# Kernel optimization log

Measured on AMD Instinct MI355X. Metric: run time of the kernel, lower is better.

Reference implementation:

```python
import jax, jax.numpy as jnp
import numpy as np

WINDOW_SIZE = 11
CHANNEL = 1
SIGMA = 1.5


def _gaussian_window(window_size=WINDOW_SIZE, channel=CHANNEL, sigma=SIGMA):
    x = np.arange(window_size)
    g = np.exp(-((x - window_size // 2) ** 2) / (2.0 * sigma ** 2))
    g = g / g.sum()
    w2d = np.outer(g, g).astype(np.float32)  # [K,K]
    # depthwise conv kernel: [C_out=channel, C_in/groups=1, K, K]
    return jnp.asarray(np.broadcast_to(w2d, (channel, 1, window_size, window_size)))


def _dwconv(x, window):
    pad = WINDOW_SIZE // 2
    return jax.lax.conv_general_dilated(
        x, window,
        window_strides=(1, 1),
        padding=[(pad, pad), (pad, pad)],
        dimension_numbers=('NCHW', 'OIHW', 'NCHW'),
        feature_group_count=CHANNEL)


def _ssim(img1, img2, window):
    C1 = 0.01 ** 2
    C2 = 0.03 ** 2
    mu1 = _dwconv(img1, window)
    mu2 = _dwconv(img2, window)
    mu1_sq = mu1 * mu1
    mu2_sq = mu2 * mu2
    mu1_mu2 = mu1 * mu2
    sigma1_sq = _dwconv(img1 * img1, window) - mu1_sq
    sigma2_sq = _dwconv(img2 * img2, window) - mu2_sq
    sigma12 = _dwconv(img1 * img2, window) - mu1_mu2
    ssim_map = ((2.0 * mu1_mu2 + C1) * (2.0 * sigma12 + C2)) / (
        (mu1_sq + mu2_sq + C1) * (sigma1_sq + sigma2_sq + C2))
    return ssim_map.mean()


def setup_inputs() -> dict:
    key = jax.random.key(0)
    k1, k2 = jax.random.split(key)
    B, C, H, W = 64, 1, 512, 512
    pred = jax.random.uniform(k1, (B, C, H, W), dtype=jnp.float32)
    target = jax.random.uniform(k2, (B, C, H, W), dtype=jnp.float32)
    return {"pred": pred, "target": target}


def reference(pred, target):
    window = _gaussian_window()
    return 1.0 - _ssim(pred[:, :1], target[:, :1], window)
```

## Files before the change

kernel.cpp:

```cpp
#include <hip/hip_runtime.h>

#define BATCH 64
#define HH 512
#define WW 512
#define TH 32
#define KS 11
#define PADK 5
#define NIN (TH + 2 * PADK)
#define NF4 262
#define NPIX (64.0 * 512.0 * 512.0)

__global__ void __launch_bounds__(256, 2) ssim_main_kernel(
    const float* __restrict__ img1, const float* __restrict__ img2,
    double* __restrict__ accum) {
  constexpr float GA[KS] = {
      0.00102838f, 0.00759884f, 0.03600087f, 0.10936069f, 0.21300553f,
      0.26601172f, 0.21300553f, 0.10936069f, 0.03600087f, 0.00759884f,
      0.00102838f};
  const float C1v = 1e-4f, C2v = 9e-4f;

  const int t  = threadIdx.x;
  const int r0 = blockIdx.x * TH;
  const int b  = blockIdx.y;

  const float2* __restrict__ pp1 =
      reinterpret_cast<const float2*>(img1 + (size_t)b * HH * WW);
  const float2* __restrict__ pp2 =
      reinterpret_cast<const float2*>(img2 + (size_t)b * HH * WW);

  __shared__ float4 sh[2][4][NF4];
  __shared__ float wsum[4];

  if (t < 6) {
    const int idx = (t < 3) ? t : (256 + t);
#pragma unroll
    for (int bi = 0; bi < 2; ++bi)
#pragma unroll
      for (int r = 0; r < 4; ++r) sh[bi][r][idx] = make_float4(0.f, 0.f, 0.f, 0.f);
  }

#define DECLR(s) float xA##s = 0.f, xB##s = 0.f, xQ##s = 0.f, xP##s = 0.f, \
                       yA##s = 0.f, yB##s = 0.f, yQ##s = 0.f, yP##s = 0.f;
  DECLR(0) DECLR(1) DECLR(2) DECLR(3) DECLR(4) DECLR(5)
  DECLR(6) DECLR(7) DECLR(8) DECLR(9) DECLR(10)

  float2 ta0, ta1, ta2, ta3, tb0, tb1, tb2, tb3;
  float local = 0.f;

#define LD1(k_, j_)                                                     \
  {                                                                     \
    constexpr int rc_ = 4 * (k_) + (j_);                                \
    ta##j_ = make_float2(0.f, 0.f);                                     \
    tb##j_ = make_float2(0.f, 0.f);                                     \
    if constexpr (rc_ < NIN) {                                          \
      const int rr_ = r0 - PADK + rc_;                                  \
      if ((unsigned)rr_ < HH) {                                         \
        const int off_ = rr_ * (WW / 2) + t;                            \
        ta##j_ = pp1[off_];                                             \
        tb##j_ = pp2[off_];                                             \
      }                                                                 \
    }                                                                   \
  }
#define LOADC(k_) { LD1(k_, 0) LD1(k_, 1) LD1(k_, 2) LD1(k_, 3) }

#define WR1(k_, j_)                                                     \
  {                                                                     \
    constexpr int rc_ = 4 * (k_) + (j_);                                \
    if constexpr (rc_ < NIN)                                            \
      sh[(k_) & 1][j_][t + 3] =                                         \
          make_float4(ta##j_.x, tb##j_.x, ta##j_.y, tb##j_.y);          \
  }
#define WRITEC(k_) { WR1(k_, 0) WR1(k_, 1) WR1(k_, 2) WR1(k_, 3) }

#define HBODY(B_, j_, S)                                                      \
  {                                                                           \
    float h0a = 0.f, h0b = 0.f, h0q = 0.f, h0p = 0.f;                         \
    float h1a = 0.f, h1b = 0.f, h1q = 0.f, h1p = 0.f;                         \
    _Pragma("unroll")                                                         \
    for (int kk = 0; kk < 7; ++kk) {                                          \
      const float4 v = sh[B_][j_][t + kk];                                    \
      if (kk >= 1) {                         \
        const float qv_ = fmaf(v.x, v.x, v.y * v.y);                          \
        const float pv_ = v.x * v.y;                                          \
        if (kk <= 5) {                                                        \
          const float w = GA[2 * kk - 1];                                     \
          h0a = fmaf(w, v.x, h0a); h0b = fmaf(w, v.y, h0b);                   \
          h0q = fmaf(w, qv_, h0q); h0p = fmaf(w, pv_, h0p);                   \
        }                                                                     \
        {                                                                     \
          const float w = GA[2 * kk - 2];                                     \
          h1a = fmaf(w, v.x, h1a); h1b = fmaf(w, v.y, h1b);                   \
          h1q = fmaf(w, qv_, h1q); h1p = fmaf(w, pv_, h1p);                   \
        }                                                                     \
      }                                                                       \
      if (kk <= 5) {                           \
        const float qv_ = fmaf(v.z, v.z, v.w * v.w);                          \
        const float pv_ = v.z * v.w;                                          \
        {                                                                     \
          const float w = GA[2 * kk];                                         \
          h0a = fmaf(w, v.z, h0a); h0b = fmaf(w, v.w, h0b);                   \
          h0q = fmaf(w, qv_, h0q); h0p = fmaf(w, pv_, h0p);                   \
        }                                                                     \
        if (kk >= 1) {                                                        \
          const float w = GA[2 * kk - 1];                                     \
          h1a = fmaf(w, v.z, h1a); h1b = fmaf(w, v.w, h1b);                   \
          h1q = fmaf(w, qv_, h1q); h1p = fmaf(w, pv_, h1p);                   \
        }                                                                     \
      }                                                                       \
    }                                                                         \
    xA##S = h0a; xB##S = h0b; xQ##S = h0q; xP##S = h0p;                       \
    yA##S = h1a; yB##S = h1b; yQ##S = h1q; yP##S = h1p;                       \
  }

#define VC(P, s0,s1,s2v,s3,s4v,s5,s6v,s7,s8,s9,s10)                           \
  fmaf(GA[10], P##s10, fmaf(GA[9], P##s9, fmaf(GA[8], P##s8,                  \
  fmaf(GA[7], P##s7, fmaf(GA[6], P##s6v, fmaf(GA[5], P##s5,                   \
  fmaf(GA[4], P##s4v, fmaf(GA[3], P##s3, fmaf(GA[2], P##s2v,                  \
  fmaf(GA[1], P##s1, GA[0] * P##s0))))))))))

#define SSIMACC                                                               \
  {                                                                           \
    const float m1s = m1 * m1, m2s = m2 * m2, m12 = m1 * m2;                  \
    const float s12 = mp - m12;                                               \
    const float sqq = mq - m1s - m2s;                                         \
    const float num = fmaf(2.f, m12, C1v) * fmaf(2.f, s12, C2v);              \
    const float den = (m1s + m2s + C1v) * (sqq + C2v);                        \
    local = fmaf(num, __builtin_amdgcn_rcpf(den), local);                     \
  }

#define VOUTBODY(s0,s1,s2v,s3,s4v,s5,s6v,s7,s8,s9,s10)                        \
  {                                                                           \
    {                                                                         \
      const float m1 = VC(xA, s0,s1,s2v,s3,s4v,s5,s6v,s7,s8,s9,s10);          \
      const float m2 = VC(xB, s0,s1,s2v,s3,s4v,s5,s6v,s7,s8,s9,s10);          \
      const float mq = VC(xQ, s0,s1,s2v,s3,s4v,s5,s6v,s7,s8,s9,s10);          \
      const float mp = VC(xP, s0,s1,s2v,s3,s4v,s5,s6v,s7,s8,s9,s10);          \
      SSIMACC                                                                 \
    }                                                                         \
    {                                                                         \
      const float m1 = VC(yA, s0,s1,s2v,s3,s4v,s5,s6v,s7,s8,s9,s10);          \
      const float m2 = VC(yB, s0,s1,s2v,s3,s4v,s5,s6v,s7,s8,s9,s10);          \
      const float mq = VC(yQ, s0,s1,s2v,s3,s4v,s5,s6v,s7,s8,s9,s10);          \
      const float mp = VC(yP, s0,s1,s2v,s3,s4v,s5,s6v,s7,s8,s9,s10);          \
      SSIMACC                                                                 \
    }                                                                         \
  }

#define ROT0  0,1,2,3,4,5,6,7,8,9,10
#define ROT1  1,2,3,4,5,6,7,8,9,10,0
#define ROT2  2,3,4,5,6,7,8,9,10,0,1
#define ROT3  3,4,5,6,7,8,9,10,0,1,2
#define ROT4  4,5,6,7,8,9,10,0,1,2,3
#define ROT5  5,6,7,8,9,10,0,1,2,3,4
#define ROT6  6,7,8,9,10,0,1,2,3,4,5
#define ROT7  7,8,9,10,0,1,2,3,4,5,6
#define ROT8  8,9,10,0,1,2,3,4,5,6,7
#define ROT9  9,10,0,1,2,3,4,5,6,7,8
#define ROT10 10,0,1,2,3,4,5,6,7,8,9
#define VOUTE(...) VOUTBODY(__VA_ARGS__)

#define ROWH(B_, j_, S)        { HBODY(B_, j_, S) }
#define ROWO(B_, j_, S, R_)    { HBODY(B_, j_, S) VOUTE(R_) }

  LOADC(0) WRITEC(0) LOADC(1)
  __syncthreads();

  WRITEC(1) LOADC(2)
  ROWH(0,0,0) ROWH(0,1,1) ROWH(0,2,2) ROWH(0,3,3)
  __syncthreads();
  WRITEC(2) LOADC(3)
  ROWH(1,0,4) ROWH(1,1,5) ROWH(1,2,6) ROWH(1,3,7)
  __syncthreads();
  WRITEC(3) LOADC(4)
  ROWH(0,0,8) ROWH(0,1,9)
  ROWO(0,2,10, ROT0) ROWO(0,3,0, ROT1)
  __syncthreads();
  WRITEC(4) LOADC(5)
  ROWO(1,0,1, ROT2) ROWO(1,1,2, ROT3) ROWO(1,2,3, ROT4) ROWO(1,3,4, ROT5)
  __syncthreads();
  WRITEC(5) LOADC(6)
  ROWO(0,0,5, ROT6) ROWO(0,1,6, ROT7) ROWO(0,2,7, ROT8) ROWO(0,3,8, ROT9)
  __syncthreads();
  WRITEC(6) LOADC(7)
  ROWO(1,0,9, ROT10) ROWO(1,1,10, ROT0) ROWO(1,2,0, ROT1) ROWO(1,3,1, ROT2)
  __syncthreads();
  WRITEC(7) LOADC(8)
  ROWO(0,0,2, ROT3) ROWO(0,1,3, ROT4) ROWO(0,2,4, ROT5) ROWO(0,3,5, ROT6)
  __syncthreads();
  WRITEC(8) LOADC(9)
  ROWO(1,0,6, ROT7) ROWO(1,1,7, ROT8) ROWO(1,2,8, ROT9) ROWO(1,3,9, ROT10)
  __syncthreads();
  WRITEC(9) LOADC(10)
  ROWO(0,0,10, ROT0) ROWO(0,1,0, ROT1) ROWO(0,2,1, ROT2) ROWO(0,3,2, ROT3)
  __syncthreads();
  WRITEC(10)
  ROWO(1,0,3, ROT4) ROWO(1,1,4, ROT5) ROWO(1,2,5, ROT6) ROWO(1,3,6, ROT7)
  __syncthreads();
  ROWO(0,0,7, ROT8) ROWO(0,1,8, ROT9)

#pragma unroll
  for (int off = 32; off > 0; off >>= 1) local += __shfl_down(local, off, 64);
  const int wave = t >> 6;
  const int lane = t & 63;
  if (lane == 0) wsum[wave] = local;
  __syncthreads();
  if (t == 0) {
    float s = wsum[0] + wsum[1] + wsum[2] + wsum[3];
    atomicAdd(accum, (double)s);
  }
}

__global__ void ssim_final_kernel(const double* __restrict__ accum,
                                  float* __restrict__ out) {
  out[0] = 1.0f - (float)(accum[0] / NPIX);
}

extern "C" void kernel_launch(void* const* d_in, const int* in_sizes, int n_in,
                              void* d_out, int out_size, void* d_ws, size_t ws_size,
                              hipStream_t stream) {
  const float* img1 = (const float*)d_in[0];
  const float* img2 = (const float*)d_in[1];
  double* accum = (double*)d_ws;
  hipMemsetAsync(accum, 0, sizeof(double), stream);

  dim3 grid(HH / TH, BATCH);
  ssim_main_kernel<<<grid, 256, 0, stream>>>(img1, img2, accum);
  ssim_final_kernel<<<1, 1, 0, stream>>>(accum, (float*)d_out);
}
```

Measured before the change: 212.2 us.

## Give each wave a private shared-memory tile with halo to drop block barriers

The shared-memory staging buffer is split into per-wave slices of 64+6 float4 entries. Six lanes per wave load and write their own halo columns. With each wave producing and consuming only its own slice, all the __syncthreads calls in the row pipeline are removed and only the final reduction barrier stays. This relies on in-order LDS access within a single wave. The cost is extra halo global loads, a slightly larger LDS footprint and extra per-lane branching.

```diff
diff --git a/kernel.cpp b/kernel.cpp
--- a/kernel.cpp
+++ b/kernel.cpp
@@ -7,7 +7,7 @@
 #define KS 11
 #define PADK 5
 #define NIN (TH + 2 * PADK)
-#define NF4 262
+#define WS4 70
 #define NPIX (64.0 * 512.0 * 512.0)
 
 __global__ void __launch_bounds__(256, 2) ssim_main_kernel(
@@ -20,6 +20,8 @@
   const float C1v = 1e-4f, C2v = 9e-4f;
 
   const int t  = threadIdx.x;
+  const int l  = t & 63;
+  const int w  = t >> 6;
   const int r0 = blockIdx.x * TH;
   const int b  = blockIdx.y;
 
@@ -28,16 +30,12 @@
   const float2* __restrict__ pp2 =
       reinterpret_cast<const float2*>(img2 + (size_t)b * HH * WW);
 
-  __shared__ float4 sh[2][4][NF4];
+  __shared__ float4 sh[4][2][4][WS4];
   __shared__ float wsum[4];
 
-  if (t < 6) {
-    const int idx = (t < 3) ? t : (256 + t);
-#pragma unroll
-    for (int bi = 0; bi < 2; ++bi)
-#pragma unroll
-      for (int r = 0; r < 4; ++r) sh[bi][r][idx] = make_float4(0.f, 0.f, 0.f, 0.f);
-  }
+  const int  hs   = (l < 3) ? l : (l + 64);
+  const int  hidx = 64 * w + hs - 3;
+  const bool hval = (l < 6) && ((unsigned)hidx < (unsigned)(WW / 2));
 
 #define DECLR(s) float xA##s = 0.f, xB##s = 0.f, xQ##s = 0.f, xP##s = 0.f, \
                        yA##s = 0.f, yB##s = 0.f, yQ##s = 0.f, yP##s = 0.f;
@@ -45,19 +43,24 @@
   DECLR(6) DECLR(7) DECLR(8) DECLR(9) DECLR(10)
 
   float2 ta0, ta1, ta2, ta3, tb0, tb1, tb2, tb3;
+  float2 ha0, ha1, ha2, ha3, hb0, hb1, hb2, hb3;
   float local = 0.f;
 
 #define LD1(k_, j_)                                                     \
   {                                                                     \
     constexpr int rc_ = 4 * (k_) + (j_);                                \
-    ta##j_ = make_float2(0.f, 0.f);                                     \
-    tb##j_ = make_float2(0.f, 0.f);                                     \
+    ta##j_ = make_float2(0.f, 0.f); tb##j_ = make_float2(0.f, 0.f);     \
+    ha##j_ = make_float2(0.f, 0.f); hb##j_ = make_float2(0.f, 0.f);     \
     if constexpr (rc_ < NIN) {                                          \
       const int rr_ = r0 - PADK + rc_;                                  \
       if ((unsigned)rr_ < HH) {                                         \
-        const int off_ = rr_ * (WW / 2) + t;                            \
-        ta##j_ = pp1[off_];                                             \
-        tb##j_ = pp2[off_];                                             \
+        const int off_ = rr_ * (WW / 2);                                \
+        ta##j_ = pp1[off_ + t];                                         \
+        tb##j_ = pp2[off_ + t];                                         \
+        if (hval) {                                                     \
+          ha##j_ = pp1[off_ + hidx];                                    \
+          hb##j_ = pp2[off_ + hidx];                                    \
+        }                                                               \
       }                                                                 \
     }                                                                   \
   }
@@ -66,9 +69,13 @@
 #define WR1(k_, j_)                                                     \
   {                                                                     \
     constexpr int rc_ = 4 * (k_) + (j_);                                \
-    if constexpr (rc_ < NIN)                                            \
-      sh[(k_) & 1][j_][t + 3] =                                         \
+    if constexpr (rc_ < NIN) {                                          \
+      sh[w][(k_) & 1][j_][l + 3] =                                      \
           make_float4(ta##j_.x, tb##j_.x, ta##j_.y, tb##j_.y);          \
+      if (l < 6)                                                        \
+        sh[w][(k_) & 1][j_][hs] =                                       \
+            make_float4(ha##j_.x, hb##j_.x, ha##j_.y, hb##j_.y);        \
+    }                                                                   \
   }
 #define WRITEC(k_) { WR1(k_, 0) WR1(k_, 1) WR1(k_, 2) WR1(k_, 3) }
 
@@ -78,33 +85,33 @@
     float h1a = 0.f, h1b = 0.f, h1q = 0.f, h1p = 0.f;                         \
     _Pragma("unroll")                                                         \
     for (int kk = 0; kk < 7; ++kk) {                                          \
-      const float4 v = sh[B_][j_][t + kk];                                    \
+      const float4 v = sh[w][B_][j_][l + kk];                                 \
       if (kk >= 1) {                         \
         const float qv_ = fmaf(v.x, v.x, v.y * v.y);                          \
         const float pv_ = v.x * v.y;                                          \
         if (kk <= 5) {                                                        \
-          const float w = GA[2 * kk - 1];                                     \
-          h0a = fmaf(w, v.x, h0a); h0b = fmaf(w, v.y, h0b);                   \
-          h0q = fmaf(w, qv_, h0q); h0p = fmaf(w, pv_, h0p);                   \
+          const float w_ = GA[2 * kk - 1];                                    \
+          h0a = fmaf(w_, v.x, h0a); h0b = fmaf(w_, v.y, h0b);                 \
+          h0q = fmaf(w_, qv_, h0q); h0p = fmaf(w_, pv_, h0p);                 \
         }                                                                     \
         {                                                                     \
-          const float w = GA[2 * kk - 2];                                     \
-          h1a = fmaf(w, v.x, h1a); h1b = fmaf(w, v.y, h1b);                   \
-          h1q = fmaf(w, qv_, h1q); h1p = fmaf(w, pv_, h1p);                   \
+          const float w_ = GA[2 * kk - 2];                                    \
+          h1a = fmaf(w_, v.x, h1a); h1b = fmaf(w_, v.y, h1b);                 \
+          h1q = fmaf(w_, qv_, h1q); h1p = fmaf(w_, pv_, h1p);                 \
         }                                                                     \
       }                                                                       \
       if (kk <= 5) {                           \
         const float qv_ = fmaf(v.z, v.z, v.w * v.w);                          \
         const float pv_ = v.z * v.w;                                          \
         {                                                                     \
-          const float w = GA[2 * kk];                                         \
-          h0a = fmaf(w, v.z, h0a); h0b = fmaf(w, v.w, h0b);                   \
-          h0q = fmaf(w, qv_, h0q); h0p = fmaf(w, pv_, h0p);                   \
+          const float w_ = GA[2 * kk];                                        \
+          h0a = fmaf(w_, v.z, h0a); h0b = fmaf(w_, v.w, h0b);                 \
+          h0q = fmaf(w_, qv_, h0q); h0p = fmaf(w_, pv_, h0p);                 \
         }                                                                     \
         if (kk >= 1) {                                                        \
-          const float w = GA[2 * kk - 1];                                     \
-          h1a = fmaf(w, v.z, h1a); h1b = fmaf(w, v.w, h1b);                   \
-          h1q = fmaf(w, qv_, h1q); h1p = fmaf(w, pv_, h1p);                   \
+          const float w_ = GA[2 * kk - 1];                                    \
+          h1a = fmaf(w_, v.z, h1a); h1b = fmaf(w_, v.w, h1b);                 \
+          h1q = fmaf(w_, qv_, h1q); h1p = fmaf(w_, pv_, h1p);                 \
         }                                                                     \
       }                                                                       \
     }                                                                         \
@@ -163,46 +170,33 @@
 #define ROWO(B_, j_, S, R_)    { HBODY(B_, j_, S) VOUTE(R_) }
 
   LOADC(0) WRITEC(0) LOADC(1)
-  __syncthreads();
 
   WRITEC(1) LOADC(2)
   ROWH(0,0,0) ROWH(0,1,1) ROWH(0,2,2) ROWH(0,3,3)
-  __syncthreads();
   WRITEC(2) LOADC(3)
   ROWH(1,0,4) ROWH(1,1,5) ROWH(1,2,6) ROWH(1,3,7)
-  __syncthreads();
   WRITEC(3) LOADC(4)
   ROWH(0,0,8) ROWH(0,1,9)
   ROWO(0,2,10, ROT0) ROWO(0,3,0, ROT1)
-  __syncthreads();
   WRITEC(4) LOADC(5)
   ROWO(1,0,1, ROT2) ROWO(1,1,2, ROT3) ROWO(1,2,3, ROT4) ROWO(1,3,4, ROT5)
-  __syncthreads();
   WRITEC(5) LOADC(6)
   ROWO(0,0,5, ROT6) ROWO(0,1,6, ROT7) ROWO(0,2,7, ROT8) ROWO(0,3,8, ROT9)
-  __syncthreads();
   WRITEC(6) LOADC(7)
   ROWO(1,0,9, ROT10) ROWO(1,1,10, ROT0) ROWO(1,2,0, ROT1) ROWO(1,3,1, ROT2)
-  __syncthreads();
   WRITEC(7) LOADC(8)
   ROWO(0,0,2, ROT3) ROWO(0,1,3, ROT4) ROWO(0,2,4, ROT5) ROWO(0,3,5, ROT6)
-  __syncthreads();
   WRITEC(8) LOADC(9)
   ROWO(1,0,6, ROT7) ROWO(1,1,7, ROT8) ROWO(1,2,8, ROT9) ROWO(1,3,9, ROT10)
-  __syncthreads();
   WRITEC(9) LOADC(10)
   ROWO(0,0,10, ROT0) ROWO(0,1,0, ROT1) ROWO(0,2,1, ROT2) ROWO(0,3,2, ROT3)
-  __syncthreads();
   WRITEC(10)
   ROWO(1,0,3, ROT4) ROWO(1,1,4, ROT5) ROWO(1,2,5, ROT6) ROWO(1,3,6, ROT7)
-  __syncthreads();
   ROWO(0,0,7, ROT8) ROWO(0,1,8, ROT9)
 
 #pragma unroll
   for (int off = 32; off > 0; off >>= 1) local += __shfl_down(local, off, 64);
-  const int wave = t >> 6;
-  const int lane = t & 63;
-  if (lane == 0) wsum[wave] = local;
+  if (l == 0) wsum[w] = local;
   __syncthreads();
   if (t == 0) {
     float s = wsum[0] + wsum[1] + wsum[2] + wsum[3];
```

Result: slower. 503.8 us (+137.4%).
